# Kernel tuning notes

Measured on AMD Instinct MI355X. Metric: run time of the kernel, lower is better.

## Reference

```python
import jax, jax.numpy as jnp
import numpy as np

EPS_VAR = 1e-10
EPS_PERP = 1e-07


def setup_inputs() -> dict:
    key = jax.random.key(0)
    k1, k2 = jax.random.split(key, 2)
    bs, dim_z, W, H, K = 64, 64, 32, 32, 1024
    z_from_encoder = jax.random.normal(k1, (bs, dim_z, W, H), dtype=jnp.float32)
    codebook = jax.random.normal(k2, (K, dim_z), dtype=jnp.float32)
    var_q = jnp.ones((1,), dtype=jnp.float32)
    return {"z_from_encoder": z_from_encoder, "var_q": var_q, "codebook": codebook}


def _vq_forward(z_from_encoder, var_q, codebook):
    bs, dim_z, W, H = z_from_encoder.shape
    K = codebook.shape[0]
    # precision = 1 / clamp(var_q, min=1e-10); gaussian_1 -> global scalar weight
    precision_q = 1.0 / jnp.clip(var_q, EPS_VAR)
    weight = (0.5 * precision_q).reshape(())  # scalar

    # [bs, dim_z, W, H] -> [N, dim_z], N = bs*W*H
    z_flat = jnp.transpose(z_from_encoder, (0, 2, 3, 1)).reshape(-1, dim_z)

    # squared euclidean distance to every code: ||z||^2 + ||c||^2 - 2 z c^T  -> [N, K]
    d2 = (jnp.sum(z_flat * z_flat, axis=1, keepdims=True)
          + jnp.sum(codebook * codebook, axis=1)
          - 2.0 * (z_flat @ codebook.T))
    logit = -(weight * d2)

    log_probs = jax.nn.log_softmax(logit, axis=-1)   # [N, K]
    probs = jnp.exp(log_probs)                        # [N, K]

    # deterministic quantization: argmax -> gather codebook (== one_hot @ codebook)
    indices = jnp.argmax(logit, axis=1)               # [N]
    z_q = codebook[indices].reshape(bs, W, H, dim_z)
    z_to_decoder = jnp.transpose(z_q, (0, 3, 1, 2))   # [bs, dim_z, W, H]

    # avg_probs = mean of hard one-hot encodings (histogram of code usage)
    N = indices.shape[0]
    avg_probs = jnp.zeros((K,), dtype=logit.dtype).at[indices].add(1.0) / N

    # kld_discrete = sum(probs * log_probs) / bs  (sum over N and K)
    kld_discrete = jnp.sum(probs * log_probs) / bs
    # kld_continuous = mean over batch of sum_i weight * (z - z_q)^2
    diff2 = (z_from_encoder - z_to_decoder) ** 2
    kld_continuous = jnp.mean(jnp.sum(weight * diff2, axis=(1, 2, 3)))
    loss = kld_discrete + kld_continuous

    perplexity = jnp.exp(-jnp.sum(avg_probs * jnp.log(avg_probs + EPS_PERP)))
    return z_to_decoder, loss, perplexity


def reference(z_from_encoder, var_q, codebook):
    return _vq_forward(z_from_encoder, var_q, codebook)
```

## Files before the change

kernel.cpp:

```cpp
#include <hip/hip_runtime.h>

#define WS_CNORM_B  512
#define WS_COUNTS_B 4608
#define WS_CBHI_B   8704
#define WS_ZERO_B   8704

typedef __attribute__((ext_vector_type(8))) short short8;
typedef __attribute__((ext_vector_type(4))) float f32x4;

__device__ __forceinline__ unsigned short f2bf(float x) {
  unsigned u = __builtin_bit_cast(unsigned, x);
  u += 0x7fffu + ((u >> 16) & 1u);
  return (unsigned short)(u >> 16);
}
__device__ __forceinline__ int qw(int r, int d) {
  return (r << 6) | (d ^ (r & 31));
}

__global__ __launch_bounds__(256) void vq_prep(const float* __restrict__ cb,
                                               char* __restrict__ ws) {
  int tid = blockIdx.x * 256 + threadIdx.x;
  int k = tid >> 6;
  float v = cb[tid];
  ((unsigned short*)(ws + WS_CBHI_B))[tid] = f2bf(v);
  float s = v * v;
  #pragma unroll
  for (int o = 32; o > 0; o >>= 1) s += __shfl_down(s, o);
  if ((threadIdx.x & 63) == 0) ((float*)(ws + WS_CNORM_B))[k] = s;
}

#define ST_OFF   16384
#define FIDX_OFF 17664

__global__ __launch_bounds__(256, 4) void vq_main(const float* __restrict__ z,
                                                  const float* __restrict__ cb,
                                                  const float* __restrict__ var_q,
                                                  char* __restrict__ ws,
                                                  float* __restrict__ out) {
  __shared__ __align__(16) char smem[17920];

  const int t = threadIdx.x;
  const int b = blockIdx.x;
  const int bb = b >> 4, p0 = (b & 15) << 6;
  const int l = t & 63, wv = t >> 6;
  const int lg = l >> 4, lr = l & 15;
  const float w = 0.5f / fmaxf(var_q[0], 1e-10f);
  const float w2 = 2.f * w;
  const float nw = -w;

  for (int i = 0; i < 8; ++i) {
    int idx = t + i * 256;
    int d2 = idx >> 6, p = idx & 63;
    float v0 = z[bb * 65536 + (2 * d2) * 1024 + p0 + p];
    float v1 = z[bb * 65536 + (2 * d2 + 1) * 1024 + p0 + p];
    unsigned short h0 = f2bf(v0), h1 = f2bf(v1);
    int byte = (p * 128 + d2 * 4) ^ ((p & 7) << 4);
    *(unsigned*)(smem + byte) = ((unsigned)h1 << 16) | h0;
  }
  __syncthreads();

  short8 a_hi[2];
  {
    int row = wv * 16 + lr;
    #pragma unroll
    for (int ks = 0; ks < 2; ++ks) {
      int byte = (row * 128 + ks * 64 + lg * 16) ^ ((row & 7) << 4);
      a_hi[ks] = *(const short8*)(smem + byte);
    }
  }
  __syncthreads();

  const char* cbh = ws + WS_CBHI_B;
  {
    #pragma unroll
    for (int pas = 0; pas < 2; ++pas) {
      int o = t + pas * 256;
      int dst = (o * 16) ^ (((o >> 3) & 7) << 4);
      *(f32x4*)(smem + dst) = *(const f32x4*)(cbh + o * 16);
    }
  }
  __syncthreads();

  float m[4], S1[4], S2[4], b1[4], b2[4];
  #pragma unroll
  for (int j = 0; j < 4; ++j) {
    m[j] = -1e30f; S1[j] = 0.f; S2[j] = 0.f; b1[j] = -1e30f; b2[j] = -1e30f;
  }

  const float* cnf = (const float*)(ws + WS_CNORM_B);

  for (int ch = 0; ch < 16; ++ch) {
    char* cur = smem + (ch & 1) * 8192;
    char* nxt = smem + ((ch + 1) & 1) * 8192;
    f32x4 rh0, rh1;
    const bool pf = ch < 15;
    if (pf) {
      const char* sh = cbh + (ch + 1) * 8192 + t * 16;
      rh0 = *(const f32x4*)sh;
      rh1 = *(const f32x4*)(sh + 4096);
    }
    float cn2[4];
    #pragma unroll
    for (int ct = 0; ct < 4; ++ct) cn2[ct] = nw * cnf[ch * 64 + ct * 16 + lr];

    f32x4 acc[4];
    #pragma unroll
    for (int ct = 0; ct < 4; ++ct) {
      f32x4 a = {};
      #pragma unroll
      for (int ks = 0; ks < 2; ++ks) {
        int cr = ct * 16 + lr;
        int byte = (cr * 128 + ks * 64 + lg * 16) ^ ((cr & 7) << 4);
        short8 bh = *(const short8*)(cur + byte);
        a = __builtin_amdgcn_mfma_f32_16x16x32_bf16(a_hi[ks], bh, a, 0, 0, 0);
      }
      acc[ct] = a;
    }

    #pragma unroll
    for (int j = 0; j < 4; ++j) {
      float lv[4];
      #pragma unroll
      for (int ct = 0; ct < 4; ++ct) lv[ct] = fmaf(acc[ct][j], w2, cn2[ct]);
      float lm = fmaxf(fmaxf(lv[0], lv[1]), fmaxf(lv[2], lv[3]));
      float mn = fmaxf(m[j], lm);
      float sc = __expf(m[j] - mn);
      S1[j] *= sc; S2[j] *= sc; m[j] = mn;
      #pragma unroll
      for (int ct = 0; ct < 4; ++ct) {
        float x = lv[ct];
        unsigned ku = (unsigned)(ch * 64 + ct * 16 + lr);
        unsigned xb = (__builtin_bit_cast(unsigned, x) & ~1023u) | ku;
        float xp = __builtin_bit_cast(float, xb);
        float tm = fminf(b1[j], xp);
        b1[j] = fmaxf(b1[j], xp);
        b2[j] = fmaxf(b2[j], tm);
        float e = __expf(x - mn);
        S1[j] += e;
        S2[j] = fmaf(x, e, S2[j]);
      }
    }

    if (pf) {
      #pragma unroll
      for (int pas = 0; pas < 2; ++pas) {
        int o = t + pas * 256;
        int dst = (o * 16) ^ (((o >> 3) & 7) << 4);
        *(f32x4*)(nxt + dst) = pas ? rh1 : rh0;
      }
    }
    __syncthreads();
  }

  #pragma unroll
  for (int st = 1; st < 16; st <<= 1) {
    #pragma unroll
    for (int j = 0; j < 4; ++j) {
      float om = __shfl_xor(m[j], st);
      float o1 = __shfl_xor(S1[j], st);
      float o2 = __shfl_xor(S2[j], st);
      float ov1 = __shfl_xor(b1[j], st);
      float ov2 = __shfl_xor(b2[j], st);
      float mn = fmaxf(m[j], om);
      float sa = __expf(m[j] - mn), sb = __expf(om - mn);
      S1[j] = sa * S1[j] + sb * o1;
      S2[j] = sa * S2[j] + sb * o2;
      m[j] = mn;
      float nb1 = fmaxf(b1[j], ov1);
      float nb2 = fmaxf(fminf(b1[j], ov1), fmaxf(b2[j], ov2));
      b1[j] = nb1; b2[j] = nb2;
    }
  }

  float* stw = (float*)(smem + ST_OFF);
  if (lr == 0) {
    #pragma unroll
    for (int j = 0; j < 4; ++j) {
      int r = wv * 16 + lg * 4 + j;
      float* p = stw + r * 5;
      p[0] = m[j]; p[1] = S1[j]; p[2] = S2[j]; p[3] = b1[j]; p[4] = b2[j];
    }
  }
  __syncthreads();

  int* fidx = (int*)(smem + FIDX_OFF);
  float rowent = 0.f, d2min = 0.f;
  if (t < 64) {
    const float* p = stw + t * 5;
    float mn = p[0], s1 = p[1], s2 = p[2];
    int ka = (int)(__builtin_bit_cast(unsigned, p[3]) & 1023u);
    int kb = (int)(__builtin_bit_cast(unsigned, p[4]) & 1023u);
    rowent = (s2 - mn * s1) / s1 - __logf(s1);
    const float* zp = z + bb * 65536 + p0 + t;
    const float* c1p = cb + ka * 64;
    const float* c2p = cb + kb * 64;
    float zn = 0.f, d1 = 0.f, d2 = 0.f;
    #pragma unroll 4
    for (int d4 = 0; d4 < 16; ++d4) {
      f32x4 ca = *(const f32x4*)(c1p + d4 * 4);
      f32x4 cc = *(const f32x4*)(c2p + d4 * 4);
      #pragma unroll
      for (int e = 0; e < 4; ++e) {
        float v = zp[(d4 * 4 + e) * 1024];
        zn = fmaf(v, v, zn);
        d1 = fmaf(v, ca[e], d1);
        d2 = fmaf(v, cc[e], d2);
      }
    }
    float da = zn + cnf[ka] - 2.f * d1;
    float db = zn + cnf[kb] - 2.f * d2;
    int kwin; float dwin;
    if (da < db || (da == db && ka < kb)) { kwin = ka; dwin = da; }
    else { kwin = kb; dwin = db; }
    fidx[t] = kwin;
    d2min = dwin;
    atomicAdd((unsigned*)(ws + WS_COUNTS_B) + kwin, 1u);
  }
  #pragma unroll
  for (int o = 32; o > 0; o >>= 1) {
    rowent += __shfl_down(rowent, o);
    d2min += __shfl_down(d2min, o);
  }
  if (t == 0) {
    float* wsf = (float*)ws;
    int slot = b & 63;
    atomicAdd(&wsf[slot * 2], rowent);
    atomicAdd(&wsf[slot * 2 + 1], d2min);
  }
  __syncthreads();

  float* zl = (float*)smem;
  for (int i = 0; i < 16; ++i) {
    int idx = t + i * 256;
    int r = idx >> 6, d = idx & 63;
    zl[qw(r, d)] = cb[fidx[r] * 64 + d];
  }
  __syncthreads();
  float* outz = out + bb * 65536 + p0;
  #pragma unroll
  for (int i = 0; i < 4; ++i) {
    int q = t + i * 256;
    int d = q >> 4, rq = q & 15, r = rq << 2;
    f32x4 v;
    v.x = zl[qw(r + 0, d)];
    v.y = zl[qw(r + 1, d)];
    v.z = zl[qw(r + 2, d)];
    v.w = zl[qw(r + 3, d)];
    *(f32x4*)&outz[d * 1024 + r] = v;
  }
}

__global__ __launch_bounds__(1024) void vq_finalize(const float* __restrict__ var_q,
                                                    char* __restrict__ ws,
                                                    float* __restrict__ out) {
  __shared__ float red[48];
  int t = threadIdx.x;
  const unsigned* counts = (const unsigned*)(ws + WS_COUNTS_B);
  const float* wsf = (const float*)ws;
  float avg = (float)counts[t] * (1.0f / 65536.0f);
  float term = avg * __logf(avg + 1e-7f);
  float pd = 0.f, pc = 0.f;
  if (t < 64) { pd = wsf[2 * t]; pc = wsf[2 * t + 1]; }
  #pragma unroll
  for (int o = 32; o > 0; o >>= 1) {
    term += __shfl_down(term, o);
    pd += __shfl_down(pd, o);
    pc += __shfl_down(pc, o);
  }
  int wv = t >> 6, lane = t & 63;
  if (lane == 0) { red[wv * 3] = term; red[wv * 3 + 1] = pd; red[wv * 3 + 2] = pc; }
  __syncthreads();
  if (t == 0) {
    float ts = 0.f, ps = 0.f, cs = 0.f;
    #pragma unroll
    for (int i = 0; i < 16; ++i) {
      ts += red[i * 3]; ps += red[i * 3 + 1]; cs += red[i * 3 + 2];
    }
    float w = 0.5f / fmaxf(var_q[0], 1e-10f);
    out[4194304] = ps / 64.f + w * cs / 64.f;
    out[4194305] = __expf(-ts);
  }
}

extern "C" void kernel_launch(void* const* d_in, const int* in_sizes, int n_in,
                              void* d_out, int out_size, void* d_ws, size_t ws_size,
                              hipStream_t stream) {
  const float* z = (const float*)d_in[0];
  const float* vq = (const float*)d_in[1];
  const float* cb = (const float*)d_in[2];
  float* out = (float*)d_out;
  char* ws = (char*)d_ws;

  hipMemsetAsync(d_ws, 0, WS_ZERO_B, stream);
  vq_prep<<<256, 256, 0, stream>>>(cb, ws);
  vq_main<<<1024, 256, 0, stream>>>(z, cb, vq, ws, out);
  vq_finalize<<<1, 1024, 0, stream>>>(vq, ws, out);
}
```

Before: 60.80 us.

## Fuse finalize into main via last-block counter and drop memset launch

Removes the workspace memset by zeroing the accumulators and a new completion counter inside the prep kernel. It also removes the separate finalize kernel: each main block bumps an atomic counter, and the last block performs the entropy and loss reduction. Codebook norms pre-scaled by -w are staged once into shared memory instead of being reloaded from global memory every chunk. The goal is to cut two launches and their inter-kernel gaps, at the cost of extra shared memory and relying on threadfence and atomic ordering for correctness.

```diff
diff --git a/kernel.cpp b/kernel.cpp
--- a/kernel.cpp
+++ b/kernel.cpp
@@ -2,8 +2,8 @@
 
 #define WS_CNORM_B  512
 #define WS_COUNTS_B 4608
-#define WS_CBHI_B   8704
-#define WS_ZERO_B   8704
+#define WS_CTR_B    8704
+#define WS_CBHI_B   8768
 
 typedef __attribute__((ext_vector_type(8))) short short8;
 typedef __attribute__((ext_vector_type(4))) float f32x4;
@@ -20,6 +20,9 @@
 __global__ __launch_bounds__(256) void vq_prep(const float* __restrict__ cb,
                                                char* __restrict__ ws) {
   int tid = blockIdx.x * 256 + threadIdx.x;
+  unsigned* w32 = (unsigned*)ws;
+  if (tid < 128) w32[tid] = 0u;
+  if (tid < 1025) w32[1152 + tid] = 0u;
   int k = tid >> 6;
   float v = cb[tid];
   ((unsigned short*)(ws + WS_CBHI_B))[tid] = f2bf(v);
@@ -31,13 +34,14 @@
 
 #define ST_OFF   16384
 #define FIDX_OFF 17664
+#define CN2L_OFF 17920
 
 __global__ __launch_bounds__(256, 4) void vq_main(const float* __restrict__ z,
                                                   const float* __restrict__ cb,
                                                   const float* __restrict__ var_q,
                                                   char* __restrict__ ws,
                                                   float* __restrict__ out) {
-  __shared__ __align__(16) char smem[17920];
+  __shared__ __align__(16) char smem[22016];
 
   const int t = threadIdx.x;
   const int b = blockIdx.x;
@@ -57,6 +61,12 @@
     int byte = (p * 128 + d2 * 4) ^ ((p & 7) << 4);
     *(unsigned*)(smem + byte) = ((unsigned)h1 << 16) | h0;
   }
+  {
+    const float* cnorm = (const float*)(ws + WS_CNORM_B);
+    float* cn2l = (float*)(smem + CN2L_OFF);
+    #pragma unroll
+    for (int i = 0; i < 4; ++i) cn2l[t + i * 256] = nw * cnorm[t + i * 256];
+  }
   __syncthreads();
 
   short8 a_hi[2];
@@ -87,7 +97,7 @@
     m[j] = -1e30f; S1[j] = 0.f; S2[j] = 0.f; b1[j] = -1e30f; b2[j] = -1e30f;
   }
 
-  const float* cnf = (const float*)(ws + WS_CNORM_B);
+  const float* cn2l = (const float*)(smem + CN2L_OFF);
 
   for (int ch = 0; ch < 16; ++ch) {
     char* cur = smem + (ch & 1) * 8192;
@@ -101,7 +111,7 @@
     }
     float cn2[4];
     #pragma unroll
-    for (int ct = 0; ct < 4; ++ct) cn2[ct] = nw * cnf[ch * 64 + ct * 16 + lr];
+    for (int ct = 0; ct < 4; ++ct) cn2[ct] = cn2l[ch * 64 + ct * 16 + lr];
 
     f32x4 acc[4];
     #pragma unroll
@@ -184,6 +194,7 @@
   __syncthreads();
 
   int* fidx = (int*)(smem + FIDX_OFF);
+  const float* cnf = (const float*)(ws + WS_CNORM_B);
   float rowent = 0.f, d2min = 0.f;
   if (t < 64) {
     const float* p = stw + t * 5;
@@ -248,37 +259,43 @@
     v.w = zl[qw(r + 3, d)];
     *(f32x4*)&outz[d * 1024 + r] = v;
   }
-}
-
-__global__ __launch_bounds__(1024) void vq_finalize(const float* __restrict__ var_q,
-                                                    char* __restrict__ ws,
-                                                    float* __restrict__ out) {
-  __shared__ float red[48];
-  int t = threadIdx.x;
-  const unsigned* counts = (const unsigned*)(ws + WS_COUNTS_B);
-  const float* wsf = (const float*)ws;
-  float avg = (float)counts[t] * (1.0f / 65536.0f);
-  float term = avg * __logf(avg + 1e-7f);
-  float pd = 0.f, pc = 0.f;
-  if (t < 64) { pd = wsf[2 * t]; pc = wsf[2 * t + 1]; }
-  #pragma unroll
-  for (int o = 32; o > 0; o >>= 1) {
-    term += __shfl_down(term, o);
-    pd += __shfl_down(pd, o);
-    pc += __shfl_down(pc, o);
-  }
-  int wv = t >> 6, lane = t & 63;
-  if (lane == 0) { red[wv * 3] = term; red[wv * 3 + 1] = pd; red[wv * 3 + 2] = pc; }
-  __syncthreads();
+
+  __syncthreads();
+  __threadfence();
+  unsigned* flag = (unsigned*)(smem + FIDX_OFF);
   if (t == 0) {
-    float ts = 0.f, ps = 0.f, cs = 0.f;
-    #pragma unroll
-    for (int i = 0; i < 16; ++i) {
-      ts += red[i * 3]; ps += red[i * 3 + 1]; cs += red[i * 3 + 2];
-    }
-    float w = 0.5f / fmaxf(var_q[0], 1e-10f);
-    out[4194304] = ps / 64.f + w * cs / 64.f;
-    out[4194305] = __expf(-ts);
+    unsigned done = atomicAdd((unsigned*)(ws + WS_CTR_B), 1u);
+    *flag = (done == 1023u) ? 1u : 0u;
+  }
+  __syncthreads();
+  if (*flag) {
+    const unsigned* counts = (const unsigned*)(ws + WS_COUNTS_B);
+    const float* wsf = (const float*)ws;
+    float term = 0.f, pd = 0.f, pc = 0.f;
+    #pragma unroll
+    for (int i = 0; i < 4; ++i) {
+      float avg = (float)counts[t + i * 256] * (1.0f / 65536.0f);
+      term += avg * __logf(avg + 1e-7f);
+    }
+    if (t < 64) { pd = wsf[2 * t]; pc = wsf[2 * t + 1]; }
+    #pragma unroll
+    for (int o = 32; o > 0; o >>= 1) {
+      term += __shfl_down(term, o);
+      pd += __shfl_down(pd, o);
+      pc += __shfl_down(pc, o);
+    }
+    float* red = (float*)(smem + ST_OFF);
+    if (l == 0) { red[wv * 3] = term; red[wv * 3 + 1] = pd; red[wv * 3 + 2] = pc; }
+    __syncthreads();
+    if (t == 0) {
+      float ts = 0.f, ps = 0.f, cs = 0.f;
+      #pragma unroll
+      for (int i = 0; i < 4; ++i) {
+        ts += red[i * 3]; ps += red[i * 3 + 1]; cs += red[i * 3 + 2];
+      }
+      out[4194304] = ps / 64.f + w * cs / 64.f;
+      out[4194305] = __expf(-ts);
+    }
   }
 }
 
@@ -291,8 +308,6 @@
   float* out = (float*)d_out;
   char* ws = (char*)d_ws;
 
-  hipMemsetAsync(d_ws, 0, WS_ZERO_B, stream);
   vq_prep<<<256, 256, 0, stream>>>(cb, ws);
   vq_main<<<1024, 256, 0, stream>>>(z, cb, vq, ws, out);
-  vq_finalize<<<1, 1024, 0, stream>>>(vq, ws, out);
-}
+}
```

After: 145.5 us. +139.4%, slower.
